# Kernel tuning notes

Hardware: AMD Instinct MI355X
Metric: run time of the kernel (lower is better)

Reference implementation:

```python
import jax, jax.numpy as jnp
import numpy as np
from jax import lax

V, T, L = 32, 8192, 16
JITTER = 1e-6
LOG2PI = float(np.log(2.0 * np.pi))


def _state_space(lengthscale, variance):
    # Matern-3/2 SDE state space: lam = sqrt(3)/ell, P0 = diag(var, var*lam^2)
    lam = jnp.sqrt(3.0) / lengthscale                      # [L]
    z = jnp.zeros_like(lam)
    P0 = jnp.stack([jnp.stack([variance, z], -1),
                    jnp.stack([z, variance * lam ** 2], -1)], -2)  # [L,2,2]
    return lam, P0


def _state_transition(dt, lam):
    # dt: [v,T,1,1,1]; lam: [L] -> A = expm(F*dt): [v,L,T,2,2]
    lam3 = lam[:, None, None]                              # [L,1,1]
    ldt = dt * lam3                                        # [v,T,L,1,1]
    e = jnp.exp(-ldt)
    a11 = e * (ldt + 1.0)
    a12 = e * jnp.broadcast_to(dt, ldt.shape)
    a21 = -e * lam3 * ldt
    a22 = e * (1.0 - ldt)
    A = jnp.concatenate([jnp.concatenate([a11, a12], -1),
                         jnp.concatenate([a21, a22], -1)], -2)  # [v,T,L,2,2]
    return jnp.swapaxes(A, 1, 2)                           # [v,L,T,2,2]


def _mT(x):
    return jnp.swapaxes(x, -1, -2)


def _update_posterior(dt_nonzero, pseudo_y, pseudo_var, lengthscale, variance):
    v, Tn, Ln = pseudo_y.shape
    dtype = pseudo_y.dtype
    lam, P0 = _state_space(lengthscale, variance)
    P0b4 = P0[:, None]                                     # [L,1,2,2]
    zeros = jnp.zeros((v, 1, 1, 1, 1), dtype)

    # ---------------- filter (dt starts with 0) ----------------
    dt_f = jnp.concatenate([zeros, dt_nonzero], axis=1)    # [v,T,1,1,1]
    A_f = _state_transition(dt_f, lam)                     # [v,L,T,2,2]
    Q_f = P0b4 - A_f @ P0b4 @ _mT(A_f)
    A_t = jnp.moveaxis(A_f, 2, 0)                          # [T,v,L,2,2]
    Q_t = jnp.moveaxis(Q_f, 2, 0)
    ys = jnp.transpose(pseudo_y, (1, 0, 2))                # [T,v,L]
    rs = jnp.transpose(pseudo_var, (1, 0, 2))
    H = jnp.array([[1.0, 0.0]], dtype=dtype)               # [1,2]

    m0 = jnp.zeros((v, Ln, 2, 1), dtype)
    P0c = jnp.broadcast_to(P0, (v, Ln, 2, 2))

    def filt_step(carry, x):
        m, P = carry
        A, Q, y, r = x                                     # A/Q: [v,L,2,2]; y/r: [v,L]
        m_p = A @ m                                        # [v,L,2,1]
        P_p = A @ P @ _mT(A) + Q                           # [v,L,2,2]
        hat = (H @ m_p)[..., 0, 0]                         # [v,L]
        HP = H @ P_p                                       # [v,L,1,2]
        s = (HP @ H.T)[..., 0, 0] + r                      # [v,L] innovation var (1x1)
        d = y - hat                                        # [v,L]
        log_p = -0.5 * (d * d / s + jnp.log(s) + LOG2PI)   # MVN(1-dim) log prob
        W = _mT(HP) / (s + JITTER)[..., None, None]        # [v,L,2,1] Kalman gain
        m_new = m_p + W * d[..., None, None]
        P_new = P_p - W @ HP
        return (m_new, P_new), (m_new, P_new, log_p)

    (_, _), (m_fs_t, P_fs_t, log_ps) = lax.scan(filt_step, (m0, P0c), (A_t, Q_t, ys, rs))
    sum_log_p = jnp.sum(log_ps, axis=(0, 2))               # sum over T then L -> [v]
    m_fs = jnp.moveaxis(m_fs_t, 0, 2)                      # [v,L,T,2,1]
    P_fs = jnp.moveaxis(P_fs_t, 0, 2)                      # [v,L,T,2,2]

    # ---------------- RTS smoother (dt ends with 0) ----------------
    dt_s = jnp.concatenate([dt_nonzero, zeros], axis=1)
    A_s = _state_transition(dt_s, lam)
    Q_s = P0b4 - A_s @ P0b4 @ _mT(A_s)
    xs = (m_fs_t, P_fs_t, jnp.moveaxis(A_s, 2, 0), jnp.moveaxis(Q_s, 2, 0))
    I2 = jnp.eye(2, dtype=dtype)

    def smooth_step(carry, x):
        m_s, P_s = carry
        m_f, P_f, A, Q = x
        m_p = A @ m_f
        A_Pf = A @ P_f
        P_p = A_Pf @ _mT(A) + Q
        G = _mT(jnp.linalg.solve(P_p + JITTER * I2, A_Pf))  # [v,L,2,2]
        m_s2 = m_f + G @ (m_s - m_p)
        P_s2 = P_f - G @ (P_s - P_p) @ _mT(G)
        mZ = (H @ m_s2)[..., 0, 0]                          # [v,L]
        PZ = (H @ P_s2 @ H.T)[..., 0, 0]                    # [v,L]
        return (m_s2, P_s2), (mZ, PZ)

    carry0 = (m_fs[:, :, -1], P_fs[:, :, -1])
    (_, _), (mZ_t, PZ_t) = lax.scan(smooth_step, carry0, xs, reverse=True)
    m_ss_Z = jnp.transpose(mZ_t, (1, 2, 0))                 # [v,L,T]
    P_ss_Z = jnp.transpose(PZ_t, (1, 2, 0))                 # [v,L,T]
    return m_fs, P_fs, m_ss_Z, P_ss_Z, sum_log_p


def setup_inputs() -> dict:
    key = jax.random.key(0)
    k1, k2, k3, k4, k5 = jax.random.split(key, 5)
    dt_nonzero = jax.random.uniform(k1, (V, T - 1, 1, 1, 1), jnp.float32) * 0.05 + 0.01
    pseudo_y = jax.random.normal(k2, (V, T, L), jnp.float32)
    pseudo_var = jax.random.uniform(k3, (V, T, L), jnp.float32) * 0.5 + 0.1
    lengthscale = jax.random.uniform(k4, (L,), jnp.float32) + 1.0
    variance = jax.random.uniform(k5, (L,), jnp.float32) * 0.5 + 0.5
    return {"dt_nonzero": dt_nonzero, "pseudo_y": pseudo_y, "pseudo_var": pseudo_var,
            "lengthscale": lengthscale, "variance": variance}


def reference(dt_nonzero, pseudo_y, pseudo_var, lengthscale, variance):
    return _update_posterior(dt_nonzero, pseudo_y, pseudo_var, lengthscale, variance)
```

## Files before the change

kernel.cpp:

```cpp
#include <hip/hip_runtime.h>

#define TV 32
#define TT 8192
#define TL 16
#define NCHAIN (TV * TL)
#define CHUNK 32
#define WARM 96
#define NCHUNK (TT / CHUNK)
#define JIT 1e-6f
#define C_LOG2PI 1.837877066409345483560659472811f
#define BF 16
#define BB 8
#define SB 8

__global__ void __launch_bounds__(256)
__attribute__((amdgpu_waves_per_eu(2, 2)))
kf_fwd(
    const float* __restrict__ dt,
    const float* __restrict__ y,
    const float* __restrict__ rvar,
    const float* __restrict__ ls,
    const float* __restrict__ var,
    float* __restrict__ m_fs,
    float* __restrict__ P_fs,
    float* __restrict__ slp,
    float4* __restrict__ g4w,
    float2* __restrict__ b2w,
    float4* __restrict__ e4w)
{
    const int tid   = blockIdx.x * 256 + threadIdx.x;
    const int chain = tid & (NCHAIN - 1);
    const int chunk = tid / NCHAIN;
    const int v = chain >> 4;
    const int l = chain & 15;

    const float lam = 1.7320508075688772f / ls[l];
    const float v0  = var[l];
    const float v1  = v0 * lam * lam;

    const int s  = chunk * CHUNK;
    const int e  = s + CHUNK;
    const int u0 = (s >= WARM) ? (s - WARM) : 0;

    const float* dtv = dt + (size_t)v * (TT - 1);
    const float* yp  = y    + (size_t)v * TT * TL + l;
    const float* rp  = rvar + (size_t)v * TT * TL + l;
    float4* mo4 = (float4*)(m_fs + (size_t)chain * TT * 2);
    float4* Po  = (float4*)(P_fs + (size_t)chain * TT * 4);

    float m0 = 0.f, m1 = 0.f;
    float P00 = v0, P01 = 0.f, P11 = v1;
    float acc = 0.f;
    float bm0 = 0.f, bm1 = 0.f;

    float gam00 = 1.f, gam01 = 0.f, gam10 = 0.f, gam11 = 1.f;
    float mbc0 = 0.f, mbc1 = 0.f;
    float me00 = 0.f, me01 = 0.f, me11 = 0.f;

    float ya[BF], ra[BF], da[BF];
    float yb[BF], rb[BF], db[BF];

#define FLOAD(Y, R, D, tb) {                                                  \
    _Pragma("unroll")                                                         \
    for (int j = 0; j < BF; ++j) {                                            \
        const int tt_ = (tb) + j;                                             \
        Y[j] = yp[(size_t)tt_ * TL];                                          \
        R[j] = rp[(size_t)tt_ * TL];                                          \
        D[j] = dtv[(tt_ >= 1) ? (tt_ - 1) : 0];                               \
    }                                                                         \
}

#define MAPCOMPOSE(SGNPLUS)                                                   \
    {                                                                         \
        const float M00_ = pp00 + JIT, M11_ = pp11 + JIT;                     \
        const float dinv_ = __builtin_amdgcn_rcpf(M00_ * M11_ - pp01 * pp01); \
        const float g00 = (M11_ * ap00 - pp01 * ap10) * dinv_;                \
        const float g01 = (-pp01 * ap00 + M00_ * ap10) * dinv_;               \
        const float g10 = (M11_ * ap01 - pp01 * ap11) * dinv_;                \
        const float g11 = (-pp01 * ap01 + M00_ * ap11) * dinv_;               \
        const float bb0 = m0 - (g00 * mp0 + g01 * mp1);                       \
        const float bb1 = m1 - (g10 * mp0 + g11 * mp1);                       \
        const float gp00 = g00 * pp00 + g01 * pp01;                           \
        const float gp01 = g00 * pp01 + g01 * pp11;                           \
        const float gp10 = g10 * pp00 + g11 * pp01;                           \
        const float gp11 = g10 * pp01 + g11 * pp11;                           \
        const float ee00 = P00 + (gp00 * g00 + gp01 * g01);                   \
        const float ee01 = P01 + (gp00 * g10 + gp01 * g11);                   \
        const float ee11 = P11 + (gp10 * g10 + gp11 * g11);                   \
        mbc0 += gam00 * bb0 + gam01 * bb1;                                    \
        mbc1 += gam10 * bb0 + gam11 * bb1;                                    \
        const float u00 = gam00 * ee00 + gam01 * ee01;                        \
        const float u01 = gam00 * ee01 + gam01 * ee11;                        \
        const float u10 = gam10 * ee00 + gam11 * ee01;                        \
        const float u11 = gam10 * ee01 + gam11 * ee11;                        \
        const float r00 = u00 * gam00 + u01 * gam01;                          \
        const float r01 = u00 * gam10 + u01 * gam11;                          \
        const float r11 = u10 * gam10 + u11 * gam11;                          \
        if (SGNPLUS) { me00 += r00; me01 += r01; me11 += r11; }               \
        else         { me00 -= r00; me01 -= r01; me11 -= r11; }               \
        const float ng00 = gam00 * g00 + gam01 * g10;                         \
        const float ng01 = gam00 * g01 + gam01 * g11;                         \
        const float ng10 = gam10 * g00 + gam11 * g10;                         \
        const float ng11 = gam10 * g01 + gam11 * g11;                         \
        gam00 = ng00; gam01 = ng01; gam10 = ng10; gam11 = ng11;               \
    }

#define FCOMP(Y, R, D, tb) {                                                  \
    _Pragma("unroll")                                                         \
    for (int j = 0; j < BF; ++j) {                                            \
        const int tt_ = (tb) + j;                                             \
        const float dtc = (tt_ == 0) ? 0.f : D[j];  \
        const float ldt = dtc * lam;                                          \
        const float ee  = __expf(-ldt);                                       \
        const float a11 = ee * (ldt + 1.f);                                   \
        const float a12 = ee * dtc;                                           \
        const float a21 = -ee * lam * ldt;                                    \
        const float a22 = ee * (1.f - ldt);                                   \
        const float q00 = v0 - (a11 * a11 * v0 + a12 * a12 * v1);             \
        const float q01 = -(a11 * a21 * v0 + a12 * a22 * v1);                 \
        const float q11 = v1 - (a21 * a21 * v0 + a22 * a22 * v1);             \
        const float mp0 = a11 * m0 + a12 * m1;                                \
        const float mp1 = a21 * m0 + a22 * m1;                                \
        const float ap00 = a11 * P00 + a12 * P01;                             \
        const float ap01 = a11 * P01 + a12 * P11;                             \
        const float ap10 = a21 * P00 + a22 * P01;                             \
        const float ap11 = a21 * P01 + a22 * P11;                             \
        const float pp00 = ap00 * a11 + ap01 * a12 + q00;                     \
        const float pp01 = ap00 * a21 + ap01 * a22 + q01;                     \
        const float pp11 = ap10 * a21 + ap11 * a22 + q11;                     \
        if (tt_ > s) MAPCOMPOSE((j & 1) != 0);            \
        const float ssv  = pp00 + R[j];                                       \
        const float d    = Y[j] - mp0;                                        \
        const float sinv = __builtin_amdgcn_rcpf(ssv + JIT);                  \
        const float W0 = pp00 * sinv;                                         \
        const float W1 = pp01 * sinv;                                         \
        m0 = mp0 + W0 * d;                                                    \
        m1 = mp1 + W1 * d;                                                    \
        P00 = pp00 - W0 * pp00;                                               \
        P01 = pp01 - W0 * pp01;                                               \
        P11 = pp11 - W1 * pp01;                                               \
        if (tt_ >= s) {            \
            acc += -0.5f * (d * d * __builtin_amdgcn_rcpf(ssv)                \
                            + __logf(ssv) + C_LOG2PI);                        \
            if ((j & 1) == 0) { bm0 = m0; bm1 = m1; }            \
            else mo4[tt_ >> 1] = make_float4(bm0, bm1, m0, m1);               \
            Po[tt_] = make_float4(P00, P01, P01, P11);                        \
        }                                                                     \
    }                                                                         \
}

    FLOAD(ya, ra, da, u0);
    __builtin_amdgcn_sched_barrier(0);
    for (int t = u0; t < e; t += 2 * BF) {
        FLOAD(yb, rb, db, t + BF);
        __builtin_amdgcn_sched_barrier(0);
        FCOMP(ya, ra, da, t);
        if (t + 2 * BF < e) {
            FLOAD(ya, ra, da, t + 2 * BF);
            __builtin_amdgcn_sched_barrier(0);
        }
        FCOMP(yb, rb, db, t + BF);
    }

    if (chunk != NCHUNK - 1) {
        const float dtc = dtv[e - 1];
        const float ldt = dtc * lam;
        const float ee  = __expf(-ldt);
        const float a11 = ee * (ldt + 1.f);
        const float a12 = ee * dtc;
        const float a21 = -ee * lam * ldt;
        const float a22 = ee * (1.f - ldt);
        const float q00 = v0 - (a11 * a11 * v0 + a12 * a12 * v1);
        const float q01 = -(a11 * a21 * v0 + a12 * a22 * v1);
        const float q11 = v1 - (a21 * a21 * v0 + a22 * a22 * v1);
        const float mp0 = a11 * m0 + a12 * m1;
        const float mp1 = a21 * m0 + a22 * m1;
        const float ap00 = a11 * P00 + a12 * P01;
        const float ap01 = a11 * P01 + a12 * P11;
        const float ap10 = a21 * P00 + a22 * P01;
        const float ap11 = a21 * P01 + a22 * P11;
        const float pp00 = ap00 * a11 + ap01 * a12 + q00;
        const float pp01 = ap00 * a21 + ap01 * a22 + q01;
        const float pp11 = ap10 * a21 + ap11 * a22 + q11;
        MAPCOMPOSE(1);
    }
    {
        const size_t mix = (size_t)chunk * NCHAIN + chain;
        g4w[mix] = make_float4(gam00, gam01, gam10, gam11);
        b2w[mix] = make_float2(mbc0, mbc1);
        e4w[mix] = make_float4(me00, me01, me11, 0.f);
    }

    for (int mask = 8; mask >= 1; mask >>= 1)
        acc += __shfl_xor(acc, mask, 16);
    if ((threadIdx.x & 15) == 0)
        atomicAdd(&slp[v], acc);
}

__global__ void __launch_bounds__(256) kf_scan(
    const float* __restrict__ m_fs,
    const float* __restrict__ P_fs,
    const float4* __restrict__ g4w,
    const float2* __restrict__ b2w,
    const float4* __restrict__ e4w,
    float2* __restrict__ xmw,
    float4* __restrict__ xPw)
{
    const int c = blockIdx.x * 256 + threadIdx.x;
    const float* mt = m_fs + ((size_t)c * TT + (TT - 1)) * 2;
    const float* Pt = P_fs + ((size_t)c * TT + (TT - 1)) * 4;
    float xm0 = mt[0], xm1 = mt[1];
    float XP00 = Pt[0], XP01 = Pt[1], XP11 = Pt[3];

    float4 Gb[SB]; float2 Bb[SB]; float4 Eb[SB];
    for (int kb = NCHUNK - 1; kb >= 0; kb -= SB) {
#pragma unroll
        for (int j = 0; j < SB; ++j) {
            const size_t ix = (size_t)(kb - j) * NCHAIN + c;
            Gb[j] = g4w[ix]; Bb[j] = b2w[ix]; Eb[j] = e4w[ix];
        }
        __builtin_amdgcn_sched_barrier(0);
#pragma unroll
        for (int j = 0; j < SB; ++j) {
            const int k = kb - j;
            const size_t ix = (size_t)k * NCHAIN + c;
            xmw[ix] = make_float2(xm0, xm1);
            xPw[ix] = make_float4(XP00, XP01, XP11, 0.f);
            const float4 G = Gb[j]; const float2 B = Bb[j]; const float4 E = Eb[j];
            const float nm0 = B.x + G.x * xm0 + G.y * xm1;
            const float nm1 = B.y + G.z * xm0 + G.w * xm1;
            const float u00 = G.x * XP00 + G.y * XP01;
            const float u01 = G.x * XP01 + G.y * XP11;
            const float u10 = G.z * XP00 + G.w * XP01;
            const float u11 = G.z * XP01 + G.w * XP11;
            const float r00 = u00 * G.x + u01 * G.y;
            const float r01 = u00 * G.z + u01 * G.w;
            const float r11 = u10 * G.z + u11 * G.w;
            xm0 = nm0; xm1 = nm1;
            if (k == NCHUNK - 1) { XP00 = E.x - r00; XP01 = E.y - r01; XP11 = E.z - r11; }
            else                 { XP00 = E.x + r00; XP01 = E.y + r01; XP11 = E.z + r11; }
        }
    }
}

__global__ void __launch_bounds__(256)
__attribute__((amdgpu_waves_per_eu(2, 2)))
kf_bwd(
    const float* __restrict__ dt,
    const float* __restrict__ ls,
    const float* __restrict__ var,
    const float* __restrict__ m_fs,
    const float* __restrict__ P_fs,
    const float2* __restrict__ xmw,
    const float4* __restrict__ xPw,
    float* __restrict__ mZ,
    float* __restrict__ PZ)
{
    const int tid   = blockIdx.x * 256 + threadIdx.x;
    const int chain = tid & (NCHAIN - 1);
    const int k     = tid / NCHAIN;
    const int v = chain >> 4;
    const int l = chain & 15;

    const float lam = 1.7320508075688772f / ls[l];
    const float v0  = var[l];
    const float v1  = v0 * lam * lam;

    const int s = k * CHUNK;
    const int e = s + CHUNK;

    const float* dtv = dt + (size_t)v * (TT - 1);
    const float2* mi  = (const float2*)(m_fs + (size_t)chain * TT * 2);
    const float4* mi4 = (const float4*)(m_fs + (size_t)chain * TT * 2);
    const float4* Pi  = (const float4*)(P_fs + (size_t)chain * TT * 4);
    float* mo = mZ + (size_t)chain * TT;
    float* Po = PZ + (size_t)chain * TT;

    const size_t mix = (size_t)k * NCHAIN + chain;
    const float2 x2 = xmw[mix];
    const float4 xq = xPw[mix];
    float ms0 = x2.x, ms1 = x2.y;
    float Ps00 = xq.x, Ps01 = xq.y, Ps11 = xq.z;

    auto step = [&](float dtc, float mf0, float mf1,
                    float Pf00, float Pf01, float Pf11) {
        const float ldt = dtc * lam;
        const float ee  = __expf(-ldt);
        const float a11 = ee * (ldt + 1.f);
        const float a12 = ee * dtc;
        const float a21 = -ee * lam * ldt;
        const float a22 = ee * (1.f - ldt);
        const float q00 = v0 - (a11 * a11 * v0 + a12 * a12 * v1);
        const float q01 = -(a11 * a21 * v0 + a12 * a22 * v1);
        const float q11 = v1 - (a21 * a21 * v0 + a22 * a22 * v1);

        const float mp0 = a11 * mf0 + a12 * mf1;
        const float mp1 = a21 * mf0 + a22 * mf1;
        const float ap00 = a11 * Pf00 + a12 * Pf01;
        const float ap01 = a11 * Pf01 + a12 * Pf11;
        const float ap10 = a21 * Pf00 + a22 * Pf01;
        const float ap11 = a21 * Pf01 + a22 * Pf11;
        const float pp00 = ap00 * a11 + ap01 * a12 + q00;
        const float pp01 = ap00 * a21 + ap01 * a22 + q01;
        const float pp11 = ap10 * a21 + ap11 * a22 + q11;

        const float M00 = pp00 + JIT, M11 = pp11 + JIT;
        const float dinv = __builtin_amdgcn_rcpf(M00 * M11 - pp01 * pp01);
        const float G00 = (M11 * ap00 - pp01 * ap10) * dinv;
        const float G01 = (-pp01 * ap00 + M00 * ap10) * dinv;
        const float G10 = (M11 * ap01 - pp01 * ap11) * dinv;
        const float G11 = (-pp01 * ap01 + M00 * ap11) * dinv;

        const float dm0 = ms0 - mp0, dm1 = ms1 - mp1;
        const float nms0 = mf0 + G00 * dm0 + G01 * dm1;
        const float nms1 = mf1 + G10 * dm0 + G11 * dm1;
        const float D00 = Ps00 - pp00, D01 = Ps01 - pp01, D11 = Ps11 - pp11;
        const float gd00 = G00 * D00 + G01 * D01;
        const float gd01 = G00 * D01 + G01 * D11;
        const float gd10 = G10 * D00 + G11 * D01;
        const float gd11 = G10 * D01 + G11 * D11;
        ms0 = nms0; ms1 = nms1;
        Ps00 = Pf00 - (gd00 * G00 + gd01 * G01);
        Ps01 = Pf01 - (gd00 * G10 + gd01 * G11);
        Ps11 = Pf11 - (gd10 * G10 + gd11 * G11);
    };

    int t;
    if (k == NCHUNK - 1) {
        mo[TT - 1] = ms0;
        Po[TT - 1] = Ps00;
        t = TT - 2;
    } else {
        t = e - 1;
    }

    for (; t >= s && (t & 7) != 7; --t) {
        const float2 mf2 = mi[t];
        const float4 Pf4 = Pi[t];
        step(dtv[t], mf2.x, mf2.y, Pf4.x, Pf4.y, Pf4.w);
        mo[t] = ms0; Po[t] = Ps00;
    }

    float b0m = 0.f, b1m = 0.f, b2m = 0.f, b3m = 0.f;
    float b0P = 0.f, b1P = 0.f, b2P = 0.f, b3P = 0.f;

    float4 Ma[BB / 2], Pa[BB]; float Da[BB];
    float4 Mb[BB / 2], Pb[BB]; float Db[BB];

#define BLOAD(M, P, D, tb) {                                                  \
    const int ib_ = ((tb) - 7) >> 1;                                          \
    _Pragma("unroll")                                                         \
    for (int j = 0; j < BB / 2; ++j) M[j] = mi4[ib_ + j];                     \
    _Pragma("unroll")                                                         \
    for (int j = 0; j < BB; ++j) {                                            \
        const int tt_ = (tb) - j;                                             \
        P[j] = Pi[tt_];                                                       \
        D[j] = dtv[tt_];                                                      \
    }                                                                         \
}

#define BCOMP(M, P, D, tb) {                                                  \
    _Pragma("unroll")                                                         \
    for (int jj = 0; jj < BB; ++jj) {                                         \
        const int tt_ = (tb) - jj;                                            \
        const int k_  = 7 - jj;             \
        const float mf0_ = (k_ & 1) ? M[k_ >> 1].z : M[k_ >> 1].x;            \
        const float mf1_ = (k_ & 1) ? M[k_ >> 1].w : M[k_ >> 1].y;            \
        step(D[jj], mf0_, mf1_, P[jj].x, P[jj].y, P[jj].w);                   \
        const int slot_ = k_ & 3;               \
        if (slot_ == 3)      { b3m = ms0; b3P = Ps00; }                       \
        else if (slot_ == 2) { b2m = ms0; b2P = Ps00; }                       \
        else if (slot_ == 1) { b1m = ms0; b1P = Ps00; }                       \
        else {                                                                \
            b0m = ms0; b0P = Ps00;                                            \
            {                                  \
                *(float4*)(mo + tt_) = make_float4(b0m, b1m, b2m, b3m);       \
                *(float4*)(Po + tt_) = make_float4(b0P, b1P, b2P, b3P);       \
            }                                                                 \
        }                                                                     \
    }                                                                         \
}

    int nb = (t - s + 1) >> 3;
    if (nb > 0) {
        BLOAD(Ma, Pa, Da, t);
        __builtin_amdgcn_sched_barrier(0);
        for (; nb >= 2; nb -= 2) {
            BLOAD(Mb, Pb, Db, t - BB);
            __builtin_amdgcn_sched_barrier(0);
            BCOMP(Ma, Pa, Da, t);
            t -= BB;
            if (nb > 2) {
                BLOAD(Ma, Pa, Da, t - BB);
                __builtin_amdgcn_sched_barrier(0);
            }
            BCOMP(Mb, Pb, Db, t);
            t -= BB;
        }
        if (nb == 1) BCOMP(Ma, Pa, Da, t);
    }
}

extern "C" void kernel_launch(void* const* d_in, const int* in_sizes, int n_in,
                              void* d_out, int out_size, void* d_ws, size_t ws_size,
                              hipStream_t stream) {
    const float* dt  = (const float*)d_in[0];
    const float* y   = (const float*)d_in[1];
    const float* rv  = (const float*)d_in[2];
    const float* ls  = (const float*)d_in[3];
    const float* var = (const float*)d_in[4];

    float* out  = (float*)d_out;
    float* m_fs = out;
    float* P_fs = m_fs + (size_t)NCHAIN * TT * 2;
    float* mZ   = P_fs + (size_t)NCHAIN * TT * 4;
    float* PZ   = mZ + (size_t)NCHAIN * TT;
    float* slp  = PZ + (size_t)NCHAIN * TT;

    float4* g4w = (float4*)d_ws;
    float4* e4w = g4w + (size_t)NCHUNK * NCHAIN;
    float4* xPw = e4w + (size_t)NCHUNK * NCHAIN;
    float2* b2w = (float2*)(xPw + (size_t)NCHUNK * NCHAIN);
    float2* xmw = b2w + (size_t)NCHUNK * NCHAIN;

    hipMemsetAsync(slp, 0, TV * sizeof(float), stream);

    const int ntask = NCHAIN * NCHUNK;
    kf_fwd<<<ntask / 256, 256, 0, stream>>>(dt, y, rv, ls, var, m_fs, P_fs, slp,
                                            g4w, b2w, e4w);
    kf_scan<<<NCHAIN / 256, 256, 0, stream>>>(m_fs, P_fs, g4w, b2w, e4w, xmw, xPw);
    kf_bwd<<<ntask / 256, 256, 0, stream>>>(dt, ls, var, m_fs, P_fs, xmw, xPw, mZ, PZ);
}
```

Baseline: 308.7 us.

## Stage y/r loads through LDS with coalesced float4 loads and double buffering

Each block now covers one chunk for 256 chains. It loads pseudo_y and pseudo_var tiles with coalesced float4 global loads into double-buffered shared memory, and dt comes in as float4 vectors. This replaces the per-thread strided scalar loads (stride of 16 floats) that wasted bandwidth and registers. The cost is __syncthreads per 16-step phase and LDS traffic. Launch bounds change from waves_per_eu to a min-blocks hint.

```diff
diff --git a/kernel.cpp b/kernel.cpp
--- a/kernel.cpp
+++ b/kernel.cpp
@@ -9,12 +9,13 @@
 #define NCHUNK (TT / CHUNK)
 #define JIT 1e-6f
 #define C_LOG2PI 1.837877066409345483560659472811f
-#define BF 16
+#define SB 8
 #define BB 8
-#define SB 8
-
-__global__ void __launch_bounds__(256)
-__attribute__((amdgpu_waves_per_eu(2, 2)))
+
+#define F4E(A, K) ((K & 3) == 0 ? A[K >> 2].x : (K & 3) == 1 ? A[K >> 2].y \
+                   : (K & 3) == 2 ? A[K >> 2].z : A[K >> 2].w)
+
+__global__ void __launch_bounds__(256, 2)
 kf_fwd(
     const float* __restrict__ dt,
     const float* __restrict__ y,
@@ -28,47 +29,68 @@
     float2* __restrict__ b2w,
     float4* __restrict__ e4w)
 {
-    const int tid   = blockIdx.x * 256 + threadIdx.x;
-    const int chain = tid & (NCHAIN - 1);
-    const int chunk = tid / NCHAIN;
+    const int tx    = threadIdx.x;
+    const int bb    = blockIdx.x;
+    const int chain = ((bb & 1) << 8) | tx;
+    const int chunk = bb >> 1;
+    const int vb    = (bb & 1) << 4;
     const int v = chain >> 4;
     const int l = chain & 15;
 
     const float lam = 1.7320508075688772f / ls[l];
-    const float v0  = var[l];
-    const float v1  = v0 * lam * lam;
+    const float pv0 = var[l];
+    const float pv1 = pv0 * lam * lam;
 
     const int s  = chunk * CHUNK;
     const int e  = s + CHUNK;
     const int u0 = (s >= WARM) ? (s - WARM) : 0;
+    const int nph = (e - u0) >> 4;
 
     const float* dtv = dt + (size_t)v * (TT - 1);
-    const float* yp  = y    + (size_t)v * TT * TL + l;
-    const float* rp  = rvar + (size_t)v * TT * TL + l;
     float4* mo4 = (float4*)(m_fs + (size_t)chain * TT * 2);
     float4* Po  = (float4*)(P_fs + (size_t)chain * TT * 4);
 
+    __shared__ float ylds[2][16][256];
+    __shared__ float rlds[2][16][256];
+
+    const int wid = tx >> 6;
+    const int q4  = (tx & 63) * 4;
+    const int svloc = q4 >> 4;
+    const int sl0   = q4 & 15;
+    const float* ysrc0 = y    + (size_t)(vb + svloc) * TT * TL + sl0;
+    const float* rsrc0 = rvar + (size_t)(vb + svloc) * TT * TL + sl0;
+
+    float4 YaA[4], RaA[4], DaA[4];
+    float4 YaB[4], RaB[4], DaB[4];
+
+#define PLOAD(YA, RA, DA, T0S) {                                              \
+    _Pragma("unroll")                                                         \
+    for (int i = 0; i < 4; ++i) {                                             \
+        const int trel = wid + 4 * i;                                         \
+        YA[i] = *(const float4*)(ysrc0 + (size_t)((T0S) + trel) * TL);        \
+        RA[i] = *(const float4*)(rsrc0 + (size_t)((T0S) + trel) * TL);        \
+        DA[i] = *(const float4*)(dtv + (T0S) + 4 * i);                        \
+    }                                                                         \
+    __builtin_amdgcn_sched_barrier(0);                                        \
+}
+
+#define PWRITE(NB, YA, RA) {                                                  \
+    _Pragma("unroll")                                                         \
+    for (int i = 0; i < 4; ++i) {                                             \
+        ((float4*)&ylds[NB][0][0])[tx + 256 * i] = YA[i];                     \
+        ((float4*)&rlds[NB][0][0])[tx + 256 * i] = RA[i];                     \
+    }                                                                         \
+}
+
     float m0 = 0.f, m1 = 0.f;
-    float P00 = v0, P01 = 0.f, P11 = v1;
+    float P00 = pv0, P01 = 0.f, P11 = pv1;
     float acc = 0.f;
     float bm0 = 0.f, bm1 = 0.f;
+    float dprev = (u0 > 0) ? dtv[u0 - 1] : 0.f;
 
     float gam00 = 1.f, gam01 = 0.f, gam10 = 0.f, gam11 = 1.f;
     float mbc0 = 0.f, mbc1 = 0.f;
     float me00 = 0.f, me01 = 0.f, me11 = 0.f;
-
-    float ya[BF], ra[BF], da[BF];
-    float yb[BF], rb[BF], db[BF];
-
-#define FLOAD(Y, R, D, tb) {                                                  \
-    _Pragma("unroll")                                                         \
-    for (int j = 0; j < BF; ++j) {                                            \
-        const int tt_ = (tb) + j;                                             \
-        Y[j] = yp[(size_t)tt_ * TL];                                          \
-        R[j] = rp[(size_t)tt_ * TL];                                          \
-        D[j] = dtv[(tt_ >= 1) ? (tt_ - 1) : 0];                               \
-    }                                                                         \
-}
 
 #define MAPCOMPOSE(SGNPLUS)                                                   \
     {                                                                         \
@@ -105,20 +127,24 @@
         gam00 = ng00; gam01 = ng01; gam10 = ng10; gam11 = ng11;               \
     }
 
-#define FCOMP(Y, R, D, tb) {                                                  \
-    _Pragma("unroll")                                                         \
-    for (int j = 0; j < BF; ++j) {                                            \
-        const int tt_ = (tb) + j;                                             \
-        const float dtc = (tt_ == 0) ? 0.f : D[j];  \
+#define PHASE(BSEL, DA, T0) {                                                 \
+    const bool wr = (T0) >= s;       \
+    _Pragma("unroll")                                                         \
+    for (int j = 0; j < 16; ++j) {                                            \
+        const int tt = (T0) + j;                                              \
+        const float yv  = ylds[BSEL][j][tx];                                  \
+        const float rvv = rlds[BSEL][j][tx];                                  \
+        const float dre = (j == 0) ? dprev : F4E(DA, ((j + 3) & 15));         \
+        const float dtc = (tt == 0) ? 0.f : dre;    \
         const float ldt = dtc * lam;                                          \
         const float ee  = __expf(-ldt);                                       \
         const float a11 = ee * (ldt + 1.f);                                   \
         const float a12 = ee * dtc;                                           \
         const float a21 = -ee * lam * ldt;                                    \
         const float a22 = ee * (1.f - ldt);                                   \
-        const float q00 = v0 - (a11 * a11 * v0 + a12 * a12 * v1);             \
-        const float q01 = -(a11 * a21 * v0 + a12 * a22 * v1);                 \
-        const float q11 = v1 - (a21 * a21 * v0 + a22 * a22 * v1);             \
+        const float q00 = pv0 - (a11 * a11 * pv0 + a12 * a12 * pv1);          \
+        const float q01 = -(a11 * a21 * pv0 + a12 * a22 * pv1);               \
+        const float q11 = pv1 - (a21 * a21 * pv0 + a22 * a22 * pv1);          \
         const float mp0 = a11 * m0 + a12 * m1;                                \
         const float mp1 = a21 * m0 + a22 * m1;                                \
         const float ap00 = a11 * P00 + a12 * P01;                             \
@@ -128,9 +154,9 @@
         const float pp00 = ap00 * a11 + ap01 * a12 + q00;                     \
         const float pp01 = ap00 * a21 + ap01 * a22 + q01;                     \
         const float pp11 = ap10 * a21 + ap11 * a22 + q11;                     \
-        if (tt_ > s) MAPCOMPOSE((j & 1) != 0);            \
-        const float ssv  = pp00 + R[j];                                       \
-        const float d    = Y[j] - mp0;                                        \
+        if (tt > s) MAPCOMPOSE((j & 1) != 0);              \
+        const float ssv  = pp00 + rvv;                                        \
+        const float d    = yv - mp0;                                          \
         const float sinv = __builtin_amdgcn_rcpf(ssv + JIT);                  \
         const float W0 = pp00 * sinv;                                         \
         const float W1 = pp01 * sinv;                                         \
@@ -139,27 +165,29 @@
         P00 = pp00 - W0 * pp00;                                               \
         P01 = pp01 - W0 * pp01;                                               \
         P11 = pp11 - W1 * pp01;                                               \
-        if (tt_ >= s) {            \
+        if (wr) {                                                             \
             acc += -0.5f * (d * d * __builtin_amdgcn_rcpf(ssv)                \
                             + __logf(ssv) + C_LOG2PI);                        \
             if ((j & 1) == 0) { bm0 = m0; bm1 = m1; }            \
-            else mo4[tt_ >> 1] = make_float4(bm0, bm1, m0, m1);               \
-            Po[tt_] = make_float4(P00, P01, P01, P11);                        \
+            else mo4[tt >> 1] = make_float4(bm0, bm1, m0, m1);                \
+            Po[tt] = make_float4(P00, P01, P01, P11);                         \
         }                                                                     \
     }                                                                         \
-}
-
-    FLOAD(ya, ra, da, u0);
-    __builtin_amdgcn_sched_barrier(0);
-    for (int t = u0; t < e; t += 2 * BF) {
-        FLOAD(yb, rb, db, t + BF);
-        __builtin_amdgcn_sched_barrier(0);
-        FCOMP(ya, ra, da, t);
-        if (t + 2 * BF < e) {
-            FLOAD(ya, ra, da, t + 2 * BF);
-            __builtin_amdgcn_sched_barrier(0);
-        }
-        FCOMP(yb, rb, db, t + BF);
+    dprev = DA[3].w;                   \
+}
+
+    PLOAD(YaA, RaA, DaA, u0);
+    PWRITE(0, YaA, RaA);
+    for (int ph = 0; ph < nph; ph += 2) {
+        const int t0 = u0 + (ph << 4);
+        __syncthreads();
+        if (ph + 1 < nph) PLOAD(YaB, RaB, DaB, t0 + 16);
+        PHASE(0, DaA, t0);
+        PWRITE(1, YaB, RaB);
+        __syncthreads();
+        if (ph + 2 < nph) PLOAD(YaA, RaA, DaA, t0 + 32);
+        PHASE(1, DaB, t0 + 16);
+        if (ph + 2 < nph) PWRITE(0, YaA, RaA);
     }
 
     if (chunk != NCHUNK - 1) {
@@ -170,9 +198,9 @@
         const float a12 = ee * dtc;
         const float a21 = -ee * lam * ldt;
         const float a22 = ee * (1.f - ldt);
-        const float q00 = v0 - (a11 * a11 * v0 + a12 * a12 * v1);
-        const float q01 = -(a11 * a21 * v0 + a12 * a22 * v1);
-        const float q11 = v1 - (a21 * a21 * v0 + a22 * a22 * v1);
+        const float q00 = pv0 - (a11 * a11 * pv0 + a12 * a12 * pv1);
+        const float q01 = -(a11 * a21 * pv0 + a12 * a22 * pv1);
+        const float q11 = pv1 - (a21 * a21 * pv0 + a22 * a22 * pv1);
         const float mp0 = a11 * m0 + a12 * m1;
         const float mp1 = a21 * m0 + a22 * m1;
         const float ap00 = a11 * P00 + a12 * P01;
@@ -193,7 +221,7 @@
 
     for (int mask = 8; mask >= 1; mask >>= 1)
         acc += __shfl_xor(acc, mask, 16);
-    if ((threadIdx.x & 15) == 0)
+    if ((tx & 15) == 0)
         atomicAdd(&slp[v], acc);
 }
 
```

Measured after the change: 336.5 us. 1.09x slower.

## Replace warm-up forward filter with exact associative-scan chunk composition

Applied to the files above, without the earlier changes.

Before, each chunk's Kalman filter started from a guessed state and ran a 96-step warm-up before its own 32 steps. Now a new kernel builds each chunk's associative filtering element (A, b, C, eta, J), and a sequential scan over chunks gives the exact starting mean and covariance for every chunk. The filter pass then runs only its own 32 steps from those states, which removes the redundant warm-up work and makes the chunk starts exact. In exchange it adds two kernel launches, a serial 256-step scan per chain, and more workspace traffic, with workspace regions reused between phases.

```diff
diff --git a/kernel.cpp b/kernel.cpp
--- a/kernel.cpp
+++ b/kernel.cpp
@@ -5,22 +5,224 @@
 #define TL 16
 #define NCHAIN (TV * TL)
 #define CHUNK 32
-#define WARM 96
 #define NCHUNK (TT / CHUNK)
+#define NE ((size_t)NCHUNK * NCHAIN)
 #define JIT 1e-6f
+#define SQ3 1.7320508075688772f
 #define C_LOG2PI 1.837877066409345483560659472811f
 #define BF 16
 #define BB 8
 #define SB 8
+#define SBF 4
+
+
+#define FLOAD(Y, R, D, tb) {                                                  \
+    _Pragma("unroll")                                                         \
+    for (int j = 0; j < BF; ++j) {                                            \
+        const int tt_ = (tb) + j;                                             \
+        Y[j] = yp[(size_t)tt_ * TL];                                          \
+        R[j] = rp[(size_t)tt_ * TL];                                          \
+        D[j] = dtv[(tt_ >= 1) ? (tt_ - 1) : 0];                               \
+    }                                                                         \
+}
+
+#define ECOMP(Y, R, D, tb, FIRSTB) {                                          \
+    _Pragma("unroll")                                                         \
+    for (int j = 0; j < BF; ++j) {                                            \
+        const int tt = (tb) + j;                                              \
+        const float dtc = (tt == 0) ? 0.f : D[j];                             \
+        const float ldt = dtc * lam;                                          \
+        const float ee  = __expf(-ldt);                                       \
+        const float a11 = ee * (ldt + 1.f);                                   \
+        const float a12 = ee * dtc;                                           \
+        const float a21 = -ee * lam * ldt;                                    \
+        const float a22 = ee * (1.f - ldt);                                   \
+        const float q00 = v0 - (a11 * a11 * v0 + a12 * a12 * v1);             \
+        const float q01 = -(a11 * a21 * v0 + a12 * a22 * v1);                 \
+        const float q11 = v1 - (a21 * a21 * v0 + a22 * a22 * v1);             \
+        const float S    = q00 + R[j];                                        \
+        const float Sinv = __builtin_amdgcn_rcpf(S);                          \
+        const float k0 = q00 * Sinv, k1 = q01 * Sinv;                         \
+        const float o0 = 1.f - k0;                                            \
+        const float sA00 = o0 * a11,        sA01 = o0 * a12;                  \
+        const float sA10 = a21 - k1 * a11,  sA11 = a22 - k1 * a12;            \
+        const float sb0 = k0 * Y[j],        sb1 = k1 * Y[j];                  \
+        const float sC00 = o0 * q00, sC01 = o0 * q01, sC11 = q11 - k1 * q01;  \
+        const float ys = Y[j] * Sinv;                                         \
+        const float sE0 = a11 * ys, sE1 = a12 * ys;                           \
+        const float sJ00 = a11 * a11 * Sinv;                                  \
+        const float sJ01 = a11 * a12 * Sinv;                                  \
+        const float sJ11 = a12 * a12 * Sinv;                                  \
+        if ((FIRSTB) && j == 0) {                                             \
+            rA00 = sA00; rA01 = sA01; rA10 = sA10; rA11 = sA11;               \
+            rb0 = sb0; rb1 = sb1;                                             \
+            rC00 = sC00; rC01 = sC01; rC11 = sC11;                            \
+            rE0 = sE0; rE1 = sE1;                                             \
+            rJ00 = sJ00; rJ01 = sJ01; rJ11 = sJ11;                            \
+        } else {                                                              \
+            const float M00 = 1.f + rC00 * sJ00 + rC01 * sJ01;                \
+            const float M01 =       rC00 * sJ01 + rC01 * sJ11;                \
+            const float M10 =       rC01 * sJ00 + rC11 * sJ01;                \
+            const float M11 = 1.f + rC01 * sJ01 + rC11 * sJ11;                \
+            const float dinv = __builtin_amdgcn_rcpf(M00 * M11 - M01 * M10);  \
+            const float N00 =  M11 * dinv, N01 = -M01 * dinv;                 \
+            const float N10 = -M10 * dinv, N11 =  M00 * dinv;                 \
+            const float T00 = sA00 * N00 + sA01 * N10;                        \
+            const float T01 = sA00 * N01 + sA01 * N11;                        \
+            const float T10 = sA10 * N00 + sA11 * N10;                        \
+            const float T11 = sA10 * N01 + sA11 * N11;                        \
+            const float U00 = rA00 * N00 + rA10 * N01;                        \
+            const float U01 = rA00 * N10 + rA10 * N11;                        \
+            const float U10 = rA01 * N00 + rA11 * N01;                        \
+            const float U11 = rA01 * N10 + rA11 * N11;                        \
+            const float u0 = rb0 + rC00 * sE0 + rC01 * sE1;                   \
+            const float u1 = rb1 + rC01 * sE0 + rC11 * sE1;                   \
+            const float nb0 = T00 * u0 + T01 * u1 + sb0;                      \
+            const float nb1 = T10 * u0 + T11 * u1 + sb1;                      \
+            const float w0 = sE0 - (sJ00 * rb0 + sJ01 * rb1);                 \
+            const float w1 = sE1 - (sJ01 * rb0 + sJ11 * rb1);                 \
+            const float nE0 = U00 * w0 + U01 * w1 + rE0;                      \
+            const float nE1 = U10 * w0 + U11 * w1 + rE1;                      \
+            const float nA00 = T00 * rA00 + T01 * rA10;                       \
+            const float nA01 = T00 * rA01 + T01 * rA11;                       \
+            const float nA10 = T10 * rA00 + T11 * rA10;                       \
+            const float nA11 = T10 * rA01 + T11 * rA11;                       \
+            const float X00 = T00 * rC00 + T01 * rC01;                        \
+            const float X01 = T00 * rC01 + T01 * rC11;                        \
+            const float X10 = T10 * rC00 + T11 * rC01;                        \
+            const float X11 = T10 * rC01 + T11 * rC11;                        \
+            const float nC00 = X00 * sA00 + X01 * sA01 + sC00;               \
+            const float nC01 = X00 * sA10 + X01 * sA11 + sC01;               \
+            const float nC11 = X10 * sA10 + X11 * sA11 + sC11;               \
+            const float V00 = sJ00 * rA00 + sJ01 * rA10;                      \
+            const float V01 = sJ00 * rA01 + sJ01 * rA11;                      \
+            const float V10 = sJ01 * rA00 + sJ11 * rA10;                      \
+            const float V11 = sJ01 * rA01 + sJ11 * rA11;                      \
+            const float nJ00 = U00 * V00 + U01 * V10 + rJ00;                  \
+            const float nJ01 = U00 * V01 + U01 * V11 + rJ01;                  \
+            const float nJ11 = U10 * V01 + U11 * V11 + rJ11;                  \
+            rA00 = nA00; rA01 = nA01; rA10 = nA10; rA11 = nA11;               \
+            rb0 = nb0; rb1 = nb1;                                             \
+            rC00 = nC00; rC01 = nC01; rC11 = nC11;                            \
+            rE0 = nE0; rE1 = nE1;                                             \
+            rJ00 = nJ00; rJ01 = nJ01; rJ11 = nJ11;                            \
+        }                                                                     \
+    }                                                                         \
+}
 
 __global__ void __launch_bounds__(256)
 __attribute__((amdgpu_waves_per_eu(2, 2)))
-kf_fwd(
+kf_f1(const float* __restrict__ dt, const float* __restrict__ y,
+      const float* __restrict__ rvar, const float* __restrict__ ls,
+      const float* __restrict__ var,
+      float4* __restrict__ eA,
+      float4* __restrict__ eC,
+      float4* __restrict__ eJ,
+      float2* __restrict__ eH)
+{
+    const int tid   = blockIdx.x * 256 + threadIdx.x;
+    const int chain = tid & (NCHAIN - 1);
+    const int k     = tid >> 9;
+    const int v = chain >> 4;
+    const int l = chain & 15;
+
+    const float lam = SQ3 / ls[l];
+    const float v0  = var[l];
+    const float v1  = v0 * lam * lam;
+    const int s = k * CHUNK;
+
+    const float* dtv = dt + (size_t)v * (TT - 1);
+    const float* yp  = y    + (size_t)v * TT * TL + l;
+    const float* rp  = rvar + (size_t)v * TT * TL + l;
+
+    float rA00, rA01, rA10, rA11, rb0, rb1;
+    float rC00, rC01, rC11, rE0, rE1, rJ00, rJ01, rJ11;
+
+    float ya[BF], ra[BF], da[BF];
+    float yb[BF], rb[BF], db[BF];
+
+    FLOAD(ya, ra, da, s);
+    __builtin_amdgcn_sched_barrier(0);
+    FLOAD(yb, rb, db, s + BF);
+    __builtin_amdgcn_sched_barrier(0);
+    ECOMP(ya, ra, da, s, 1);
+    ECOMP(yb, rb, db, s + BF, 0);
+
+    const size_t ix = (size_t)k * NCHAIN + chain;
+    eA[ix] = make_float4(rA00, rA01, rA10, rA11);
+    eC[ix] = make_float4(rC00, rC01, rC11, rb0);
+    eJ[ix] = make_float4(rJ00, rJ01, rJ11, rb1);
+    eH[ix] = make_float2(rE0, rE1);
+}
+
+__global__ void __launch_bounds__(256) kf_scanF(
+    const float* __restrict__ ls, const float* __restrict__ var,
+    const float4* __restrict__ eA, const float4* __restrict__ eC,
+    const float4* __restrict__ eJ, const float2* __restrict__ eH,
+    float2* __restrict__ xmF, float4* __restrict__ xPF)
+{
+    const int c = blockIdx.x * 256 + threadIdx.x;
+    const int l = c & 15;
+    const float lam = SQ3 / ls[l];
+    const float v0 = var[l];
+    const float v1 = v0 * lam * lam;
+
+    float m0 = 0.f, m1 = 0.f;
+    float P00 = v0, P01 = 0.f, P11 = v1;
+
+    float4 Aa[SBF], Ca[SBF], Ja[SBF]; float2 Ha[SBF];
+
+    for (int kb = 0; kb < NCHUNK; kb += SBF) {
+#pragma unroll
+        for (int j = 0; j < SBF; ++j) {
+            const size_t ix = (size_t)(kb + j) * NCHAIN + c;
+            Aa[j] = eA[ix]; Ca[j] = eC[ix]; Ja[j] = eJ[ix]; Ha[j] = eH[ix];
+        }
+        __builtin_amdgcn_sched_barrier(0);
+#pragma unroll
+        for (int j = 0; j < SBF; ++j) {
+            const size_t ix = (size_t)(kb + j) * NCHAIN + c;
+            xmF[ix] = make_float2(m0, m1);
+            xPF[ix] = make_float4(P00, P01, P11, 0.f);
+            const float4 A = Aa[j]; const float4 C = Ca[j];
+            const float4 J = Ja[j]; const float2 H = Ha[j];
+            const float M00 = 1.f + P00 * J.x + P01 * J.y;
+            const float M01 =       P00 * J.y + P01 * J.z;
+            const float M10 =       P01 * J.x + P11 * J.y;
+            const float M11 = 1.f + P01 * J.y + P11 * J.z;
+            const float dinv = __builtin_amdgcn_rcpf(M00 * M11 - M01 * M10);
+            const float N00 =  M11 * dinv, N01 = -M01 * dinv;
+            const float N10 = -M10 * dinv, N11 =  M00 * dinv;
+            const float W00 = A.x * N00 + A.y * N10;
+            const float W01 = A.x * N01 + A.y * N11;
+            const float W10 = A.z * N00 + A.w * N10;
+            const float W11 = A.z * N01 + A.w * N11;
+            const float u0 = m0 + P00 * H.x + P01 * H.y;
+            const float u1 = m1 + P01 * H.x + P11 * H.y;
+            const float nm0 = W00 * u0 + W01 * u1 + C.w;
+            const float nm1 = W10 * u0 + W11 * u1 + J.w;
+            const float X00 = W00 * P00 + W01 * P01;
+            const float X01 = W00 * P01 + W01 * P11;
+            const float X10 = W10 * P00 + W11 * P01;
+            const float X11 = W10 * P01 + W11 * P11;
+            P00 = X00 * A.x + X01 * A.y + C.x;
+            P01 = X00 * A.z + X01 * A.w + C.y;
+            P11 = X10 * A.z + X11 * A.w + C.z;
+            m0 = nm0; m1 = nm1;
+        }
+    }
+}
+
+__global__ void __launch_bounds__(256)
+__attribute__((amdgpu_waves_per_eu(2, 2)))
+kf_f2(
     const float* __restrict__ dt,
     const float* __restrict__ y,
     const float* __restrict__ rvar,
     const float* __restrict__ ls,
     const float* __restrict__ var,
+    const float2* __restrict__ xmF,
+    const float4* __restrict__ xPF,
     float* __restrict__ m_fs,
     float* __restrict__ P_fs,
     float* __restrict__ slp,
@@ -34,13 +236,12 @@
     const int v = chain >> 4;
     const int l = chain & 15;
 
-    const float lam = 1.7320508075688772f / ls[l];
+    const float lam = SQ3 / ls[l];
     const float v0  = var[l];
     const float v1  = v0 * lam * lam;
 
     const int s  = chunk * CHUNK;
     const int e  = s + CHUNK;
-    const int u0 = (s >= WARM) ? (s - WARM) : 0;
 
     const float* dtv = dt + (size_t)v * (TT - 1);
     const float* yp  = y    + (size_t)v * TT * TL + l;
@@ -48,10 +249,14 @@
     float4* mo4 = (float4*)(m_fs + (size_t)chain * TT * 2);
     float4* Po  = (float4*)(P_fs + (size_t)chain * TT * 4);
 
-    float m0 = 0.f, m1 = 0.f;
-    float P00 = v0, P01 = 0.f, P11 = v1;
+    const size_t mix = (size_t)chunk * NCHAIN + chain;
+    const float2 bmx = xmF[mix];
+    const float4 bPx = xPF[mix];
+    float m0 = bmx.x, m1 = bmx.y;
+    float P00 = bPx.x, P01 = bPx.y, P11 = bPx.z;
     float acc = 0.f;
     float bm0 = 0.f, bm1 = 0.f;
+    float pe0 = 0.f, pe1 = 0.f, pe2 = 0.f;
 
     float gam00 = 1.f, gam01 = 0.f, gam10 = 0.f, gam11 = 1.f;
     float mbc0 = 0.f, mbc1 = 0.f;
@@ -59,16 +264,6 @@
 
     float ya[BF], ra[BF], da[BF];
     float yb[BF], rb[BF], db[BF];
-
-#define FLOAD(Y, R, D, tb) {                                                  \
-    _Pragma("unroll")                                                         \
-    for (int j = 0; j < BF; ++j) {                                            \
-        const int tt_ = (tb) + j;                                             \
-        Y[j] = yp[(size_t)tt_ * TL];                                          \
-        R[j] = rp[(size_t)tt_ * TL];                                          \
-        D[j] = dtv[(tt_ >= 1) ? (tt_ - 1) : 0];                               \
-    }                                                                         \
-}
 
 #define MAPCOMPOSE(SGNPLUS)                                                   \
     {                                                                         \
@@ -139,28 +334,27 @@
         P00 = pp00 - W0 * pp00;                                               \
         P01 = pp01 - W0 * pp01;                                               \
         P11 = pp11 - W1 * pp01;                                               \
-        if (tt_ >= s) {            \
+        {                                                                     \
             acc += -0.5f * (d * d * __builtin_amdgcn_rcpf(ssv)                \
                             + __logf(ssv) + C_LOG2PI);                        \
-            if ((j & 1) == 0) { bm0 = m0; bm1 = m1; }            \
-            else mo4[tt_ >> 1] = make_float4(bm0, bm1, m0, m1);               \
-            Po[tt_] = make_float4(P00, P01, P01, P11);                        \
+            if ((j & 1) == 0) {                   \
+                bm0 = m0; bm1 = m1;                                           \
+                pe0 = P00; pe1 = P01; pe2 = P11;                              \
+            } else {                          \
+                mo4[tt_ >> 1] = make_float4(bm0, bm1, m0, m1);                \
+                Po[tt_ - 1] = make_float4(pe0, pe1, pe1, pe2);                \
+                Po[tt_]     = make_float4(P00, P01, P01, P11);                \
+            }                                                                 \
         }                                                                     \
     }                                                                         \
 }
 
-    FLOAD(ya, ra, da, u0);
+    FLOAD(ya, ra, da, s);
     __builtin_amdgcn_sched_barrier(0);
-    for (int t = u0; t < e; t += 2 * BF) {
-        FLOAD(yb, rb, db, t + BF);
-        __builtin_amdgcn_sched_barrier(0);
-        FCOMP(ya, ra, da, t);
-        if (t + 2 * BF < e) {
-            FLOAD(ya, ra, da, t + 2 * BF);
-            __builtin_amdgcn_sched_barrier(0);
-        }
-        FCOMP(yb, rb, db, t + BF);
-    }
+    FLOAD(yb, rb, db, s + BF);
+    __builtin_amdgcn_sched_barrier(0);
+    FCOMP(ya, ra, da, s);
+    FCOMP(yb, rb, db, s + BF);
 
     if (chunk != NCHUNK - 1) {
         const float dtc = dtv[e - 1];
@@ -185,7 +379,6 @@
         MAPCOMPOSE(1);
     }
     {
-        const size_t mix = (size_t)chunk * NCHAIN + chain;
         g4w[mix] = make_float4(gam00, gam01, gam10, gam11);
         b2w[mix] = make_float2(mbc0, mbc1);
         e4w[mix] = make_float4(me00, me01, me11, 0.f);
@@ -197,7 +390,7 @@
         atomicAdd(&slp[v], acc);
 }
 
-__global__ void __launch_bounds__(256) kf_scan(
+__global__ void __launch_bounds__(256) kf_scanB(
     const float* __restrict__ m_fs,
     const float* __restrict__ P_fs,
     const float4* __restrict__ g4w,
@@ -262,7 +455,7 @@
     const int v = chain >> 4;
     const int l = chain & 15;
 
-    const float lam = 1.7320508075688772f / ls[l];
+    const float lam = SQ3 / ls[l];
     const float v0  = var[l];
     const float v1  = v0 * lam * lam;
 
@@ -417,17 +610,27 @@
     float* PZ   = mZ + (size_t)NCHAIN * TT;
     float* slp  = PZ + (size_t)NCHAIN * TT;
 
-    float4* g4w = (float4*)d_ws;
-    float4* e4w = g4w + (size_t)NCHUNK * NCHAIN;
-    float4* xPw = e4w + (size_t)NCHUNK * NCHAIN;
-    float2* b2w = (float2*)(xPw + (size_t)NCHUNK * NCHAIN);
-    float2* xmw = b2w + (size_t)NCHUNK * NCHAIN;
+    float* base = (float*)d_ws;
+    float4* eA = (float4*)base;
+    float4* eC = (float4*)(base + NE * 4);
+    float4* eJ = (float4*)(base + NE * 8);
+    float2* eH = (float2*)(base + NE * 12);
+    float4* g4w = (float4*)base;
+    float4* e4w = (float4*)(base + NE * 4);
+    float2* b2w = (float2*)(base + NE * 8);
+    float* R2 = base + NE * 14;
+    float2* xmF = (float2*)R2;
+    float4* xPF = (float4*)(R2 + NE * 2);
+    float2* xmw = xmF;
+    float4* xPw = xPF;
 
     hipMemsetAsync(slp, 0, TV * sizeof(float), stream);
 
     const int ntask = NCHAIN * NCHUNK;
-    kf_fwd<<<ntask / 256, 256, 0, stream>>>(dt, y, rv, ls, var, m_fs, P_fs, slp,
-                                            g4w, b2w, e4w);
-    kf_scan<<<NCHAIN / 256, 256, 0, stream>>>(m_fs, P_fs, g4w, b2w, e4w, xmw, xPw);
+    kf_f1<<<ntask / 256, 256, 0, stream>>>(dt, y, rv, ls, var, eA, eC, eJ, eH);
+    kf_scanF<<<NCHAIN / 256, 256, 0, stream>>>(ls, var, eA, eC, eJ, eH, xmF, xPF);
+    kf_f2<<<ntask / 256, 256, 0, stream>>>(dt, y, rv, ls, var, xmF, xPF,
+                                           m_fs, P_fs, slp, g4w, b2w, e4w);
+    kf_scanB<<<NCHAIN / 256, 256, 0, stream>>>(m_fs, P_fs, g4w, b2w, e4w, xmw, xPw);
     kf_bwd<<<ntask / 256, 256, 0, stream>>>(dt, ls, var, m_fs, P_fs, xmw, xPw, mZ, PZ);
 }
```

Measured after the change: 687.6 us. 2.23x slower.
